# Optimization experiments

Measured on AMD Instinct MI355X. Metric: run time of the kernel, lower is better.

Reference implementation:

```python
import jax, jax.numpy as jnp
import numpy as np

T, B, D = 2048, 16, 1024


def setup_inputs() -> dict:
    key = jax.random.key(0)
    ks = jax.random.split(key, 8)
    std = 1.0 / D ** 0.5
    x = jax.random.normal(ks[0], (T, B, D), dtype=jnp.float32)
    h0 = jnp.zeros((B, D), dtype=jnp.float32)
    Wx = jax.random.uniform(ks[1], (D, D), jnp.float32, -std, std)
    R = jax.random.uniform(ks[2], (D, D), jnp.float32, -std, std)
    bias = jnp.zeros((D,), dtype=jnp.float32)
    W_delta = jax.random.uniform(ks[3], (D, D), jnp.float32, -std * 0.1, std * 0.1)
    b_delta = jnp.full((D,), 3.0, dtype=jnp.float32)  # delta_init
    A = jax.random.uniform(ks[4], (D,), jnp.float32, -0.5, 0.5)  # A_init_range
    W_gate_x = jax.random.uniform(ks[5], (D, D), jnp.float32, -std, std)
    W_gate_h = jax.random.uniform(ks[6], (D, D), jnp.float32, -std, std)
    b_gate = jnp.zeros((D,), dtype=jnp.float32)
    return {"x": x, "h0": h0, "Wx": Wx, "R": R, "bias": bias,
            "W_delta": W_delta, "b_delta": b_delta, "A": A,
            "W_gate_x": W_gate_x, "W_gate_h": W_gate_h, "b_gate": b_gate}


def reference(x, h0, Wx, R, bias, W_delta, b_delta, A, W_gate_x, W_gate_h, b_gate):
    # Input-dependent timestep: dt = softplus(x @ W_delta^T + b_delta), [T,B,D]
    dt = jax.nn.softplus(jnp.einsum('tbd,ed->tbe', x, W_delta) + b_delta)
    # Mamba-style log parameterization: decay_rate in (0,1), alpha in (0,1)
    decay_rate = jnp.exp(-jnp.exp(A))                 # [D]
    alpha = jnp.exp(-dt * decay_rate)                 # [T,B,D]
    # Precompute input projection once (big GEMM outside the scan)
    wx = jnp.einsum('tbd,ed->tbe', x, Wx) + bias      # [T,B,D]

    def step(h, inp):
        wx_t, a_t = inp                               # [B,D], [B,D]
        cand = jnp.tanh(h @ R.T + wx_t)               # nonlinear candidate
        h_new = a_t * h + (1.0 - a_t) * cand          # exponential blend
        return h_new, h_new

    _, h_out = jax.lax.scan(step, h0, (wx, alpha))    # h_out: [T,B,D] == h[1:]

    # h+x selective output gate
    gate_raw = (jnp.einsum('tbd,ed->tbe', x, W_gate_x)
                + jnp.einsum('tbd,ed->tbe', h_out, W_gate_h) + b_gate)
    return h_out * jax.nn.silu(gate_raw)
```

## Files before the change

### kernel.cpp

```cpp
#include <hip/hip_runtime.h>
#include <cstdint>
#include <cstddef>

typedef _Float16 f16;
typedef _Float16 f16x8 __attribute__((ext_vector_type(8)));
typedef _Float16 f16x4v __attribute__((ext_vector_type(4)));
typedef float f32x4 __attribute__((ext_vector_type(4)));
typedef unsigned uint2v __attribute__((ext_vector_type(2)));

#define TT 2048
#define BB 16
#define DD 1024
#define MM (TT*BB)
#define FPAD 16

__global__ void cvt_kernel(const float* __restrict__ in, f16* __restrict__ out, int n4){
  int stride = gridDim.x * blockDim.x;
  for (int j = blockIdx.x*blockDim.x + threadIdx.x; j < n4; j += stride){
    float4 v = ((const float4*)in)[j];
    f16x4v o;
    o[0]=(f16)v.x; o[1]=(f16)v.y; o[2]=(f16)v.z; o[3]=(f16)v.w;
    ((f16x4v*)out)[j] = o;
  }
}

__global__ void cvt5_kernel(const float* __restrict__ a0, const float* __restrict__ a1,
                            const float* __restrict__ a2, const float* __restrict__ a3,
                            const float* __restrict__ a4,
                            f16* __restrict__ o0, f16* __restrict__ o1,
                            f16* __restrict__ o2, f16* __restrict__ o3, f16* __restrict__ o4){
  const float* src[5] = {a0,a1,a2,a3,a4};
  f16* dst[5] = {o0,o1,o2,o3,o4};
  int which = blockIdx.y;
  const float* in = src[which];
  f16* out = dst[which];
  int j = blockIdx.x*blockDim.x + threadIdx.x;
  float4 v = ((const float4*)in)[j];
  f16x4v o;
  o[0]=(f16)v.x; o[1]=(f16)v.y; o[2]=(f16)v.z; o[3]=(f16)v.w;
  ((f16x4v*)out)[j] = o;
}

__global__ void init_rec_kernel(const float* __restrict__ h0, f16* __restrict__ hbuf,
                                unsigned* __restrict__ flags){
  int tid = blockIdx.x*blockDim.x + threadIdx.x;
  if (tid < 64*FPAD) flags[tid] = 0u;
  if (tid < BB*DD) hbuf[tid] = (f16)h0[tid];
}

#define GEMM_PROLOGUE() \
  __shared__ f16 As[128*32]; \
  __shared__ f16 Bs[128*32]; \
  int tid = threadIdx.x; \
  int l = tid & 63, w = tid >> 6; \
  int wr = w >> 1, wc = w & 1; \
  f32x4 acc[4][4]; \
  _Pragma("unroll") for (int i=0;i<4;++i) _Pragma("unroll") for (int jj=0;jj<4;++jj) \
    acc[i][jj] = (f32x4){0.f,0.f,0.f,0.f};

#define GEMM_KSTEP(Asrc, Bsrc, ktl) { \
  __syncthreads(); \
  _Pragma("unroll") for (int hh=0; hh<2; ++hh){ \
    int r = hh*64 + (tid>>2); \
    int q = (tid&3) ^ (r&3); \
    const f16* ga = (Asrc) + (size_t)(bm*128+r)*DD + (ktl)*32 + q*8; \
    const f16* gb = (Bsrc) + (size_t)(bcol*128+r)*DD + (ktl)*32 + q*8; \
    __builtin_amdgcn_global_load_lds((__attribute__((address_space(1))) void*)ga, \
        (__attribute__((address_space(3))) void*)(As + hh*2048 + tid*8), 16, 0, 0); \
    __builtin_amdgcn_global_load_lds((__attribute__((address_space(1))) void*)gb, \
        (__attribute__((address_space(3))) void*)(Bs + hh*2048 + tid*8), 16, 0, 0); \
  } \
  __syncthreads(); \
  int lr = l & 15, g = l >> 4; \
  f16x8 af[4], bf[4]; \
  _Pragma("unroll") for (int i=0;i<4;++i){ \
    int Ra = wr*64 + i*16 + lr; \
    int Rb = wc*64 + i*16 + lr; \
    af[i] = *(const f16x8*)(As + Ra*32 + ((g ^ (Ra & 3)) * 8)); \
    bf[i] = *(const f16x8*)(Bs + Rb*32 + ((g ^ (Rb & 3)) * 8)); \
  } \
  _Pragma("unroll") for (int i=0;i<4;++i) \
    _Pragma("unroll") for (int jj=0;jj<4;++jj) \
      acc[i][jj] = __builtin_amdgcn_mfma_f32_16x16x32_f16(af[i], bf[jj], acc[i][jj], 0,0,0); \
}

__global__ __launch_bounds__(256)
void gemm_wa_kernel(const f16* __restrict__ x16,
                    const f16* __restrict__ Wx16, const f16* __restrict__ Wd16,
                    f16* __restrict__ wxo, f16* __restrict__ alo,
                    const float* __restrict__ bias, const float* __restrict__ bd,
                    const float* __restrict__ Aar)
{
  int bm = blockIdx.x, bn = blockIdx.y;
  int alpha_path = (bn >= 8);
  int bcol = bn & 7;
  const f16* Bw = alpha_path ? Wd16 : Wx16;

  GEMM_PROLOGUE();
  for (int kt = 0; kt < 32; ++kt) GEMM_KSTEP(x16, Bw, kt);

  int lr = l & 15, lh = l >> 4;
  #pragma unroll
  for (int i=0;i<4;++i){
    #pragma unroll
    for (int jj=0;jj<4;++jj){
      #pragma unroll
      for (int r=0;r<4;++r){
        int row = bm*128 + wr*64 + i*16 + lh*4 + r;
        int col = bcol*128 + wc*64 + jj*16 + lr;
        float v = acc[i][jj][r];
        size_t off = (size_t)row*DD + col;
        if (!alpha_path){
          wxo[off] = (f16)(v + bias[col]);
        } else {
          float pre = v + bd[col];
          float sp  = (pre > 20.f) ? pre : log1pf(expf(pre));
          float decay = expf(-expf(Aar[col]));
          alo[off] = (f16)expf(-sp*decay);
        }
      }
    }
  }
}

__global__ __launch_bounds__(256)
void gemm_fin_kernel(const f16* __restrict__ hout16, const f16* __restrict__ x16,
                     const f16* __restrict__ Wgh16, const f16* __restrict__ Wgx16,
                     float* __restrict__ out, const float* __restrict__ bg)
{
  int bm = blockIdx.x, bcol = blockIdx.y;

  GEMM_PROLOGUE();
  for (int kt = 0; kt < 32; ++kt) GEMM_KSTEP(hout16, Wgh16, kt);
  for (int kt = 0; kt < 32; ++kt) GEMM_KSTEP(x16,    Wgx16, kt);

  int lr = l & 15, lh = l >> 4;
  #pragma unroll
  for (int i=0;i<4;++i){
    #pragma unroll
    for (int jj=0;jj<4;++jj){
      #pragma unroll
      for (int r=0;r<4;++r){
        int row = bm*128 + wr*64 + i*16 + lh*4 + r;
        int col = bcol*128 + wc*64 + jj*16 + lr;
        float g = acc[i][jj][r] + bg[col];
        size_t off = (size_t)row*DD + col;
        float hval = (float)hout16[off];
        out[off] = hval * g / (1.f + expf(-g));
      }
    }
  }
}

__global__ __launch_bounds__(64)
void rec_kernel(const f16* __restrict__ Rf, const f16* __restrict__ wx,
                const f16* __restrict__ alpha, const float* __restrict__ h0,
                f16* __restrict__ hbuf, f16* __restrict__ hout,
                unsigned* __restrict__ flags)
{
  __shared__ f16 Rlds[32*64*8];

  int l = threadIdx.x;
  int j = blockIdx.x;
  int e0 = j * 16;

  #pragma unroll
  for (int kt=0; kt<32; ++kt){
    int e = e0 + (l & 15);
    int d = kt*32 + (l >> 4)*8;
    *(uint4*)(Rlds + ((size_t)kt*64 + l)*8) = *(const uint4*)(Rf + (size_t)e*DD + d);
  }

  int b = l & 15, rr0 = (l >> 4) * 4;
  float4 hstate = *(const float4*)(h0 + (size_t)b*DD + e0 + rr0);
  __syncthreads();

  f32x4 wxv, alv;
  {
    f16x4v wh = *(const f16x4v*)(wx + (size_t)b*DD + e0 + rr0);
    f16x4v ah = *(const f16x4v*)(alpha + (size_t)b*DD + e0 + rr0);
    #pragma unroll
    for (int r=0;r<4;++r){ wxv[r] = (float)wh[r]; alv[r] = (float)ah[r]; }
  }

  for (int t = 0; t < TT; ++t){
    if (t > 0){
      const unsigned* fp = flags + l*FPAD;
      int guard = 0;
      unsigned long long notready = 1ull;
      while (notready && guard < 2000000){
        unsigned fv = __hip_atomic_load(fp, __ATOMIC_RELAXED, __HIP_MEMORY_SCOPE_AGENT);
        notready = __ballot(fv < (unsigned)t);
        ++guard;
        if (notready && guard > 16) __builtin_amdgcn_s_sleep(1);
      }
    }

    const f16* hb = hbuf + (size_t)(t & 1) * (BB*DD);
    f16x8 hfr[32];
    #pragma unroll
    for (int kt=0; kt<32; ++kt){
      const f16* hp = hb + (size_t)b*DD + kt*32 + (l >> 4)*8;
      asm volatile("global_load_dwordx4 %0, %1, off sc0 sc1"
                   : "=v"(hfr[kt]) : "v"(hp) : "memory");
    }

    f32x4 accv[4];
    #pragma unroll
    for (int c=0;c<4;++c) accv[c] = (f32x4){0.f,0.f,0.f,0.f};

    asm volatile("s_waitcnt vmcnt(24)" ::: "memory");
    __builtin_amdgcn_sched_barrier(0);
    #pragma unroll
    for (int kt=0; kt<8; ++kt){
      f16x8 a = *(const f16x8*)(Rlds + ((size_t)kt*64 + l)*8);
      accv[kt&3] = __builtin_amdgcn_mfma_f32_16x16x32_f16(a, hfr[kt], accv[kt&3], 0, 0, 0);
    }
    asm volatile("s_waitcnt vmcnt(16)" ::: "memory");
    __builtin_amdgcn_sched_barrier(0);
    #pragma unroll
    for (int kt=8; kt<16; ++kt){
      f16x8 a = *(const f16x8*)(Rlds + ((size_t)kt*64 + l)*8);
      accv[kt&3] = __builtin_amdgcn_mfma_f32_16x16x32_f16(a, hfr[kt], accv[kt&3], 0, 0, 0);
    }
    asm volatile("s_waitcnt vmcnt(8)" ::: "memory");
    __builtin_amdgcn_sched_barrier(0);

    int tn = (t+1 < TT) ? (t+1) : t;
    size_t offn = ((size_t)tn*BB + b)*DD + e0 + rr0;
    f16x4v whn = *(const f16x4v*)(wx + offn);
    f16x4v ahn = *(const f16x4v*)(alpha + offn);

    #pragma unroll
    for (int kt=16; kt<24; ++kt){
      f16x8 a = *(const f16x8*)(Rlds + ((size_t)kt*64 + l)*8);
      accv[kt&3] = __builtin_amdgcn_mfma_f32_16x16x32_f16(a, hfr[kt], accv[kt&3], 0, 0, 0);
    }
    asm volatile("s_waitcnt vmcnt(0)" ::: "memory");
    __builtin_amdgcn_sched_barrier(0);
    #pragma unroll
    for (int kt=24; kt<32; ++kt){
      f16x8 a = *(const f16x8*)(Rlds + ((size_t)kt*64 + l)*8);
      accv[kt&3] = __builtin_amdgcn_mfma_f32_16x16x32_f16(a, hfr[kt], accv[kt&3], 0, 0, 0);
    }
    f32x4 acc = (accv[0]+accv[1]) + (accv[2]+accv[3]);

    f16x4v h4;
    float hs[4] = {hstate.x, hstate.y, hstate.z, hstate.w};
    #pragma unroll
    for (int r=0;r<4;++r){
      float z = acc[r] + wxv[r];
      float cand = tanhf(z);
      float hn = alv[r]*hs[r] + (1.f - alv[r])*cand;
      hs[r] = hn;
      h4[r] = (f16)hn;
    }
    hstate = (float4){hs[0], hs[1], hs[2], hs[3]};

    f16* hw = hbuf + (size_t)((t+1) & 1) * (BB*DD) + (size_t)b*DD + e0 + rr0;
    uint2v hv = __builtin_bit_cast(uint2v, h4);
    asm volatile("global_store_dwordx2 %0, %1, off sc0 sc1"
                 :: "v"(hw), "v"(hv) : "memory");
    asm volatile("s_waitcnt vmcnt(0)" ::: "memory");
    if (l == 0)
      __hip_atomic_store(flags + j*FPAD, (unsigned)(t+1),
                         __ATOMIC_RELAXED, __HIP_MEMORY_SCOPE_AGENT);

    *(f16x4v*)(hout + ((size_t)t*BB + b)*DD + e0 + rr0) = h4;
    #pragma unroll
    for (int r=0;r<4;++r){ wxv[r] = (float)whn[r]; alv[r] = (float)ahn[r]; }
  }
}

extern "C" void kernel_launch(void* const* d_in, const int* in_sizes, int n_in,
                              void* d_out, int out_size, void* d_ws, size_t ws_size,
                              hipStream_t stream)
{
  const float* x    = (const float*)d_in[0];
  const float* h0   = (const float*)d_in[1];
  const float* Wx   = (const float*)d_in[2];
  const float* R    = (const float*)d_in[3];
  const float* bias = (const float*)d_in[4];
  const float* Wd   = (const float*)d_in[5];
  const float* bd   = (const float*)d_in[6];
  const float* Aar  = (const float*)d_in[7];
  const float* Wgx  = (const float*)d_in[8];
  const float* Wgh  = (const float*)d_in[9];
  const float* bg   = (const float*)d_in[10];
  float* out = (float*)d_out;

  char* ws = (char*)d_ws;
  size_t off = 0;
  auto carve = [&](size_t bytes) -> void* {
    void* p = ws + off;
    off += (bytes + 255) & ~(size_t)255;
    return p;
  };
  f16* x16    = (f16*)carve((size_t)MM*DD*2);
  f16* Wx16   = (f16*)carve((size_t)DD*DD*2);
  f16* Wd16   = (f16*)carve((size_t)DD*DD*2);
  f16* Wgx16  = (f16*)carve((size_t)DD*DD*2);
  f16* Wgh16  = (f16*)carve((size_t)DD*DD*2);
  f16* R16    = (f16*)carve((size_t)DD*DD*2);
  f16* wx16   = (f16*)carve((size_t)MM*DD*2);
  f16* al16   = (f16*)carve((size_t)MM*DD*2);
  f16* hout16 = (f16*)carve((size_t)MM*DD*2);
  f16* hbuf   = (f16*)carve((size_t)2*BB*DD*2);
  unsigned* flags = (unsigned*)carve(64*FPAD*4);
  if (off > ws_size) return;

  cvt_kernel<<<1024, 256, 0, stream>>>(x, x16, MM*DD/4);
  dim3 g5(DD*DD/4/256, 5);
  cvt5_kernel<<<g5, 256, 0, stream>>>(Wx, Wd, Wgx, Wgh, R,
                                      Wx16, Wd16, Wgx16, Wgh16, R16);
  init_rec_kernel<<<64, 256, 0, stream>>>(h0, hbuf, flags);

  dim3 gwa(MM/128, 16);
  gemm_wa_kernel<<<gwa, 256, 0, stream>>>(x16, Wx16, Wd16, wx16, al16, bias, bd, Aar);

  rec_kernel<<<64, 64, 0, stream>>>(R16, wx16, al16, h0, hbuf, hout16, flags);

  dim3 gfin(MM/128, DD/128);
  gemm_fin_kernel<<<gfin, 256, 0, stream>>>(hout16, x16, Wgh16, Wgx16, out, bg);
}
```

Before: 7.009 ms.

## Fuse recurrence with output-gate GEMM using persistent tile workers gated on progress

Merges the sequential recurrence kernel and the final gate GEMM into one launch. 64 blocks run the scan and publish a global step counter, while 192 persistent blocks pull output tiles from an atomic queue and start each tile once the rows of h it needs have been written. This overlaps the final GEMM with the latency-bound recurrence instead of running it afterwards. The cost is extra coherent (sc0 sc1) loads of hout, spin-waiting workers that may compete with the recurrence blocks for memory and CU resources, and a dependence on all blocks being co-resident.

Result: slower. 7.400 ms (+5.6%).

```diff
diff --git a/kernel.cpp b/kernel.cpp
--- a/kernel.cpp
+++ b/kernel.cpp
@@ -13,6 +13,10 @@
 #define DD 1024
 #define MM (TT*BB)
 #define FPAD 16
+#define NFIN 192
+
+#define AS1 __attribute__((address_space(1)))
+#define AS3 __attribute__((address_space(3)))
 
 __global__ void cvt_kernel(const float* __restrict__ in, f16* __restrict__ out, int n4){
   int stride = gridDim.x * blockDim.x;
@@ -44,7 +48,7 @@
 __global__ void init_rec_kernel(const float* __restrict__ h0, f16* __restrict__ hbuf,
                                 unsigned* __restrict__ flags){
   int tid = blockIdx.x*blockDim.x + threadIdx.x;
-  if (tid < 64*FPAD) flags[tid] = 0u;
+  if (tid < 64*FPAD + 64) flags[tid] = 0u;
   if (tid < BB*DD) hbuf[tid] = (f16)h0[tid];
 }
 
@@ -65,10 +69,8 @@
     int q = (tid&3) ^ (r&3); \
     const f16* ga = (Asrc) + (size_t)(bm*128+r)*DD + (ktl)*32 + q*8; \
     const f16* gb = (Bsrc) + (size_t)(bcol*128+r)*DD + (ktl)*32 + q*8; \
-    __builtin_amdgcn_global_load_lds((__attribute__((address_space(1))) void*)ga, \
-        (__attribute__((address_space(3))) void*)(As + hh*2048 + tid*8), 16, 0, 0); \
-    __builtin_amdgcn_global_load_lds((__attribute__((address_space(1))) void*)gb, \
-        (__attribute__((address_space(3))) void*)(Bs + hh*2048 + tid*8), 16, 0, 0); \
+    __builtin_amdgcn_global_load_lds((AS1 void*)ga, (AS3 void*)(As + hh*2048 + tid*8), 16, 0, 0); \
+    __builtin_amdgcn_global_load_lds((AS1 void*)gb, (AS3 void*)(Bs + hh*2048 + tid*8), 16, 0, 0); \
   } \
   __syncthreads(); \
   int lr = l & 15, g = l >> 4; \
@@ -124,151 +126,277 @@
 }
 
 __global__ __launch_bounds__(256)
-void gemm_fin_kernel(const f16* __restrict__ hout16, const f16* __restrict__ x16,
-                     const f16* __restrict__ Wgh16, const f16* __restrict__ Wgx16,
-                     float* __restrict__ out, const float* __restrict__ bg)
+void recfin_kernel(const f16* __restrict__ Rf, const f16* __restrict__ wx,
+                   const f16* __restrict__ alpha, const float* __restrict__ h0,
+                   f16* __restrict__ hbuf, f16* __restrict__ hout,
+                   unsigned* __restrict__ flags, unsigned* __restrict__ gstep,
+                   unsigned* __restrict__ wcnt,
+                   const f16* __restrict__ x16, const f16* __restrict__ Wgh16,
+                   const f16* __restrict__ Wgx16, float* __restrict__ out,
+                   const float* __restrict__ bg)
 {
-  int bm = blockIdx.x, bcol = blockIdx.y;
-
-  GEMM_PROLOGUE();
-  for (int kt = 0; kt < 32; ++kt) GEMM_KSTEP(hout16, Wgh16, kt);
-  for (int kt = 0; kt < 32; ++kt) GEMM_KSTEP(x16,    Wgx16, kt);
-
-  int lr = l & 15, lh = l >> 4;
-  #pragma unroll
-  for (int i=0;i<4;++i){
+  __shared__ __align__(16) char smem[32768];
+  __shared__ unsigned tilevar;
+
+  if (blockIdx.x < 64){
+    if (threadIdx.x >= 64) return;
+    f16* Rlds = (f16*)smem;
+    int l = threadIdx.x;
+    int j = blockIdx.x;
+    int e0 = j * 16;
+
     #pragma unroll
-    for (int jj=0;jj<4;++jj){
+    for (int kt=0; kt<32; ++kt){
+      int e = e0 + (l & 15);
+      int d = kt*32 + (l >> 4)*8;
+      *(uint4*)(Rlds + ((size_t)kt*64 + l)*8) = *(const uint4*)(Rf + (size_t)e*DD + d);
+    }
+    asm volatile("s_waitcnt lgkmcnt(0)" ::: "memory");
+    __builtin_amdgcn_sched_barrier(0);
+
+    int b = l & 15, rr0 = (l >> 4) * 4;
+    float4 hstate = *(const float4*)(h0 + (size_t)b*DD + e0 + rr0);
+
+    f32x4 wxv, alv;
+    {
+      f16x4v wh = *(const f16x4v*)(wx + (size_t)b*DD + e0 + rr0);
+      f16x4v ah = *(const f16x4v*)(alpha + (size_t)b*DD + e0 + rr0);
+      #pragma unroll
+      for (int r=0;r<4;++r){ wxv[r] = (float)wh[r]; alv[r] = (float)ah[r]; }
+    }
+
+    for (int t = 0; t < TT; ++t){
+      if (t > 0){
+        const unsigned* fp = flags + l*FPAD;
+        int guard = 0;
+        unsigned long long notready = 1ull;
+        while (notready && guard < 2000000){
+          unsigned fv = __hip_atomic_load(fp, __ATOMIC_RELAXED, __HIP_MEMORY_SCOPE_AGENT);
+          notready = __ballot(fv < (unsigned)t);
+          ++guard;
+          if (notready && guard > 16) __builtin_amdgcn_s_sleep(1);
+        }
+        if (j == 0 && l == 0)
+          __hip_atomic_store(gstep, (unsigned)t, __ATOMIC_RELAXED, __HIP_MEMORY_SCOPE_AGENT);
+      }
+
+      const f16* hb = hbuf + (size_t)(t & 1) * (BB*DD);
+      f16x8 hfr[32];
+      #pragma unroll
+      for (int kt=0; kt<32; ++kt){
+        const f16* hp = hb + (size_t)b*DD + kt*32 + (l >> 4)*8;
+        asm volatile("global_load_dwordx4 %0, %1, off sc0 sc1"
+                     : "=v"(hfr[kt]) : "v"(hp) : "memory");
+      }
+
+      f32x4 accv[4];
+      #pragma unroll
+      for (int c=0;c<4;++c) accv[c] = (f32x4){0.f,0.f,0.f,0.f};
+
+      asm volatile("s_waitcnt vmcnt(24)" ::: "memory");
+      __builtin_amdgcn_sched_barrier(0);
+      #pragma unroll
+      for (int kt=0; kt<8; ++kt){
+        f16x8 a = *(const f16x8*)(Rlds + ((size_t)kt*64 + l)*8);
+        accv[kt&3] = __builtin_amdgcn_mfma_f32_16x16x32_f16(a, hfr[kt], accv[kt&3], 0, 0, 0);
+      }
+      asm volatile("s_waitcnt vmcnt(16)" ::: "memory");
+      __builtin_amdgcn_sched_barrier(0);
+      #pragma unroll
+      for (int kt=8; kt<16; ++kt){
+        f16x8 a = *(const f16x8*)(Rlds + ((size_t)kt*64 + l)*8);
+        accv[kt&3] = __builtin_amdgcn_mfma_f32_16x16x32_f16(a, hfr[kt], accv[kt&3], 0, 0, 0);
+      }
+      asm volatile("s_waitcnt vmcnt(8)" ::: "memory");
+      __builtin_amdgcn_sched_barrier(0);
+
+      int tn = (t+1 < TT) ? (t+1) : t;
+      size_t offn = ((size_t)tn*BB + b)*DD + e0 + rr0;
+      f16x4v whn = *(const f16x4v*)(wx + offn);
+      f16x4v ahn = *(const f16x4v*)(alpha + offn);
+
+      #pragma unroll
+      for (int kt=16; kt<24; ++kt){
+        f16x8 a = *(const f16x8*)(Rlds + ((size_t)kt*64 + l)*8);
+        accv[kt&3] = __builtin_amdgcn_mfma_f32_16x16x32_f16(a, hfr[kt], accv[kt&3], 0, 0, 0);
+      }
+      asm volatile("s_waitcnt vmcnt(0)" ::: "memory");
+      __builtin_amdgcn_sched_barrier(0);
+      #pragma unroll
+      for (int kt=24; kt<32; ++kt){
+        f16x8 a = *(const f16x8*)(Rlds + ((size_t)kt*64 + l)*8);
+        accv[kt&3] = __builtin_amdgcn_mfma_f32_16x16x32_f16(a, hfr[kt], accv[kt&3], 0, 0, 0);
+      }
+      f32x4 acc = (accv[0]+accv[1]) + (accv[2]+accv[3]);
+
+      f16x4v h4;
+      float hs[4] = {hstate.x, hstate.y, hstate.z, hstate.w};
       #pragma unroll
       for (int r=0;r<4;++r){
-        int row = bm*128 + wr*64 + i*16 + lh*4 + r;
-        int col = bcol*128 + wc*64 + jj*16 + lr;
-        float g = acc[i][jj][r] + bg[col];
-        size_t off = (size_t)row*DD + col;
-        float hval = (float)hout16[off];
-        out[off] = hval * g / (1.f + expf(-g));
-      }
-    }
-  }
-}
-
-__global__ __launch_bounds__(64)
-void rec_kernel(const f16* __restrict__ Rf, const f16* __restrict__ wx,
-                const f16* __restrict__ alpha, const float* __restrict__ h0,
-                f16* __restrict__ hbuf, f16* __restrict__ hout,
-                unsigned* __restrict__ flags)
-{
-  __shared__ f16 Rlds[32*64*8];
-
-  int l = threadIdx.x;
-  int j = blockIdx.x;
-  int e0 = j * 16;
-
-  #pragma unroll
-  for (int kt=0; kt<32; ++kt){
-    int e = e0 + (l & 15);
-    int d = kt*32 + (l >> 4)*8;
-    *(uint4*)(Rlds + ((size_t)kt*64 + l)*8) = *(const uint4*)(Rf + (size_t)e*DD + d);
-  }
-
-  int b = l & 15, rr0 = (l >> 4) * 4;
-  float4 hstate = *(const float4*)(h0 + (size_t)b*DD + e0 + rr0);
-  __syncthreads();
-
-  f32x4 wxv, alv;
-  {
-    f16x4v wh = *(const f16x4v*)(wx + (size_t)b*DD + e0 + rr0);
-    f16x4v ah = *(const f16x4v*)(alpha + (size_t)b*DD + e0 + rr0);
-    #pragma unroll
-    for (int r=0;r<4;++r){ wxv[r] = (float)wh[r]; alv[r] = (float)ah[r]; }
-  }
-
-  for (int t = 0; t < TT; ++t){
-    if (t > 0){
+        float z = acc[r] + wxv[r];
+        float cand = tanhf(z);
+        float hn = alv[r]*hs[r] + (1.f - alv[r])*cand;
+        hs[r] = hn;
+        h4[r] = (f16)hn;
+      }
+      hstate = (float4){hs[0], hs[1], hs[2], hs[3]};
+
+      f16* hw = hbuf + (size_t)((t+1) & 1) * (BB*DD) + (size_t)b*DD + e0 + rr0;
+      uint2v hv = __builtin_bit_cast(uint2v, h4);
+      asm volatile("global_store_dwordx2 %0, %1, off sc0 sc1"
+                   :: "v"(hw), "v"(hv) : "memory");
+      f16* hop = hout + ((size_t)t*BB + b)*DD + e0 + rr0;
+      asm volatile("global_store_dwordx2 %0, %1, off sc0 sc1"
+                   :: "v"(hop), "v"(hv) : "memory");
+      asm volatile("s_waitcnt vmcnt(0)" ::: "memory");
+      if (l == 0)
+        __hip_atomic_store(flags + j*FPAD, (unsigned)(t+1),
+                           __ATOMIC_RELAXED, __HIP_MEMORY_SCOPE_AGENT);
+
+      #pragma unroll
+      for (int r=0;r<4;++r){ wxv[r] = (float)whn[r]; alv[r] = (float)ahn[r]; }
+    }
+
+    if (j == 0){
       const unsigned* fp = flags + l*FPAD;
       int guard = 0;
       unsigned long long notready = 1ull;
       while (notready && guard < 2000000){
         unsigned fv = __hip_atomic_load(fp, __ATOMIC_RELAXED, __HIP_MEMORY_SCOPE_AGENT);
-        notready = __ballot(fv < (unsigned)t);
+        notready = __ballot(fv < 2048u);
         ++guard;
-        if (notready && guard > 16) __builtin_amdgcn_s_sleep(1);
-      }
-    }
-
-    const f16* hb = hbuf + (size_t)(t & 1) * (BB*DD);
-    f16x8 hfr[32];
+        if (notready) __builtin_amdgcn_s_sleep(1);
+      }
+      if (l == 0)
+        __hip_atomic_store(gstep, 2048u, __ATOMIC_RELAXED, __HIP_MEMORY_SCOPE_AGENT);
+    }
+    return;
+  }
+
+  f16* As = (f16*)smem;
+  f16* Bs = (f16*)(smem + 8192);
+  int tid = threadIdx.x;
+  int l = tid & 63, w = tid >> 6;
+  int wr = w >> 1, wc = w & 1;
+  int lr = l & 15, lh = l >> 4;
+
+  for (;;){
+    if (tid == 0) tilevar = atomicAdd(wcnt, 1u);
+    __syncthreads();
+    unsigned g = tilevar;
+    __syncthreads();
+    if (g >= 2048u) break;
+    int bm = (int)(g >> 3), bcol = (int)(g & 7);
+
+    if (tid == 0){
+      unsigned need = (unsigned)((bm + 1) * 8);
+      int guard = 0;
+      while (guard < 1000000){
+        unsigned gs = __hip_atomic_load(gstep, __ATOMIC_RELAXED, __HIP_MEMORY_SCOPE_AGENT);
+        if (gs >= need) break;
+        ++guard;
+        __builtin_amdgcn_s_sleep(32);
+      }
+    }
+    __syncthreads();
+
+    f32x4 acc[4][4];
     #pragma unroll
-    for (int kt=0; kt<32; ++kt){
-      const f16* hp = hb + (size_t)b*DD + kt*32 + (l >> 4)*8;
-      asm volatile("global_load_dwordx4 %0, %1, off sc0 sc1"
-                   : "=v"(hfr[kt]) : "v"(hp) : "memory");
-    }
-
-    f32x4 accv[4];
+    for (int i=0;i<4;++i)
+      #pragma unroll
+      for (int jj=0;jj<4;++jj)
+        acc[i][jj] = (f32x4){0.f,0.f,0.f,0.f};
+
+    for (int kt = 0; kt < 32; ++kt){
+      __syncthreads();
+      int r0_ = tid >> 2,        q0 = (tid & 3) ^ (r0_ & 3);
+      int r1_ = 64 + (tid >> 2), q1 = (tid & 3) ^ (r1_ & 3);
+      f16x8 va0, va1;
+      const f16* ga0 = hout + (size_t)(bm*128 + r0_)*DD + kt*32 + q0*8;
+      const f16* ga1 = hout + (size_t)(bm*128 + r1_)*DD + kt*32 + q1*8;
+      asm volatile("global_load_dwordx4 %0, %1, off sc0 sc1" : "=v"(va0) : "v"(ga0) : "memory");
+      asm volatile("global_load_dwordx4 %0, %1, off sc0 sc1" : "=v"(va1) : "v"(ga1) : "memory");
+      const f16* gb0 = Wgh16 + (size_t)(bcol*128 + r0_)*DD + kt*32 + q0*8;
+      const f16* gb1 = Wgh16 + (size_t)(bcol*128 + r1_)*DD + kt*32 + q1*8;
+      __builtin_amdgcn_global_load_lds((AS1 void*)gb0, (AS3 void*)(Bs + tid*8), 16, 0, 0);
+      __builtin_amdgcn_global_load_lds((AS1 void*)gb1, (AS3 void*)(Bs + 2048 + tid*8), 16, 0, 0);
+      asm volatile("s_waitcnt vmcnt(0)" ::: "memory");
+      __builtin_amdgcn_sched_barrier(0);
+      *(f16x8*)(As + tid*8) = va0;
+      *(f16x8*)(As + 2048 + tid*8) = va1;
+      __syncthreads();
+      f16x8 af[4], bf[4];
+      #pragma unroll
+      for (int i=0;i<4;++i){
+        int Ra = wr*64 + i*16 + lr;
+        int Rb = wc*64 + i*16 + lr;
+        af[i] = *(const f16x8*)(As + Ra*32 + ((lh ^ (Ra & 3)) * 8));
+        bf[i] = *(const f16x8*)(Bs + Rb*32 + ((lh ^ (Rb & 3)) * 8));
+      }
+      #pragma unroll
+      for (int i=0;i<4;++i)
+        #pragma unroll
+        for (int jj=0;jj<4;++jj)
+          acc[i][jj] = __builtin_amdgcn_mfma_f32_16x16x32_f16(af[i], bf[jj], acc[i][jj], 0,0,0);
+    }
+
+    for (int kt = 0; kt < 32; ++kt){
+      __syncthreads();
+      #pragma unroll
+      for (int hh=0; hh<2; ++hh){
+        int r = hh*64 + (tid>>2);
+        int q = (tid&3) ^ (r&3);
+        const f16* ga = x16   + (size_t)(bm*128+r)*DD + kt*32 + q*8;
+        const f16* gb = Wgx16 + (size_t)(bcol*128+r)*DD + kt*32 + q*8;
+        __builtin_amdgcn_global_load_lds((AS1 void*)ga, (AS3 void*)(As + hh*2048 + tid*8), 16, 0, 0);
+        __builtin_amdgcn_global_load_lds((AS1 void*)gb, (AS3 void*)(Bs + hh*2048 + tid*8), 16, 0, 0);
+      }
+      __syncthreads();
+      f16x8 af[4], bf[4];
+      #pragma unroll
+      for (int i=0;i<4;++i){
+        int Ra = wr*64 + i*16 + lr;
+        int Rb = wc*64 + i*16 + lr;
+        af[i] = *(const f16x8*)(As + Ra*32 + ((lh ^ (Ra & 3)) * 8));
+        bf[i] = *(const f16x8*)(Bs + Rb*32 + ((lh ^ (Rb & 3)) * 8));
+      }
+      #pragma unroll
+      for (int i=0;i<4;++i)
+        #pragma unroll
+        for (int jj=0;jj<4;++jj)
+          acc[i][jj] = __builtin_amdgcn_mfma_f32_16x16x32_f16(af[i], bf[jj], acc[i][jj], 0,0,0);
+    }
+
+    unsigned hvr[4][4][4];
     #pragma unroll
-    for (int c=0;c<4;++c) accv[c] = (f32x4){0.f,0.f,0.f,0.f};
-
-    asm volatile("s_waitcnt vmcnt(24)" ::: "memory");
-    __builtin_amdgcn_sched_barrier(0);
-    #pragma unroll
-    for (int kt=0; kt<8; ++kt){
-      f16x8 a = *(const f16x8*)(Rlds + ((size_t)kt*64 + l)*8);
-      accv[kt&3] = __builtin_amdgcn_mfma_f32_16x16x32_f16(a, hfr[kt], accv[kt&3], 0, 0, 0);
-    }
-    asm volatile("s_waitcnt vmcnt(16)" ::: "memory");
-    __builtin_amdgcn_sched_barrier(0);
-    #pragma unroll
-    for (int kt=8; kt<16; ++kt){
-      f16x8 a = *(const f16x8*)(Rlds + ((size_t)kt*64 + l)*8);
-      accv[kt&3] = __builtin_amdgcn_mfma_f32_16x16x32_f16(a, hfr[kt], accv[kt&3], 0, 0, 0);
-    }
-    asm volatile("s_waitcnt vmcnt(8)" ::: "memory");
-    __builtin_amdgcn_sched_barrier(0);
-
-    int tn = (t+1 < TT) ? (t+1) : t;
-    size_t offn = ((size_t)tn*BB + b)*DD + e0 + rr0;
-    f16x4v whn = *(const f16x4v*)(wx + offn);
-    f16x4v ahn = *(const f16x4v*)(alpha + offn);
-
-    #pragma unroll
-    for (int kt=16; kt<24; ++kt){
-      f16x8 a = *(const f16x8*)(Rlds + ((size_t)kt*64 + l)*8);
-      accv[kt&3] = __builtin_amdgcn_mfma_f32_16x16x32_f16(a, hfr[kt], accv[kt&3], 0, 0, 0);
-    }
+    for (int i=0;i<4;++i)
+      #pragma unroll
+      for (int jj=0;jj<4;++jj)
+        #pragma unroll
+        for (int r=0;r<4;++r){
+          const f16* hp = hout + (size_t)(bm*128 + wr*64 + i*16 + lh*4 + r)*DD
+                               + bcol*128 + wc*64 + jj*16 + lr;
+          asm volatile("global_load_ushort %0, %1, off sc0 sc1"
+                       : "=v"(hvr[i][jj][r]) : "v"(hp) : "memory");
+        }
     asm volatile("s_waitcnt vmcnt(0)" ::: "memory");
     __builtin_amdgcn_sched_barrier(0);
+
     #pragma unroll
-    for (int kt=24; kt<32; ++kt){
-      f16x8 a = *(const f16x8*)(Rlds + ((size_t)kt*64 + l)*8);
-      accv[kt&3] = __builtin_amdgcn_mfma_f32_16x16x32_f16(a, hfr[kt], accv[kt&3], 0, 0, 0);
-    }
-    f32x4 acc = (accv[0]+accv[1]) + (accv[2]+accv[3]);
-
-    f16x4v h4;
-    float hs[4] = {hstate.x, hstate.y, hstate.z, hstate.w};
-    #pragma unroll
-    for (int r=0;r<4;++r){
-      float z = acc[r] + wxv[r];
-      float cand = tanhf(z);
-      float hn = alv[r]*hs[r] + (1.f - alv[r])*cand;
-      hs[r] = hn;
-      h4[r] = (f16)hn;
-    }
-    hstate = (float4){hs[0], hs[1], hs[2], hs[3]};
-
-    f16* hw = hbuf + (size_t)((t+1) & 1) * (BB*DD) + (size_t)b*DD + e0 + rr0;
-    uint2v hv = __builtin_bit_cast(uint2v, h4);
-    asm volatile("global_store_dwordx2 %0, %1, off sc0 sc1"
-                 :: "v"(hw), "v"(hv) : "memory");
-    asm volatile("s_waitcnt vmcnt(0)" ::: "memory");
-    if (l == 0)
-      __hip_atomic_store(flags + j*FPAD, (unsigned)(t+1),
-                         __ATOMIC_RELAXED, __HIP_MEMORY_SCOPE_AGENT);
-
-    *(f16x4v*)(hout + ((size_t)t*BB + b)*DD + e0 + rr0) = h4;
-    #pragma unroll
-    for (int r=0;r<4;++r){ wxv[r] = (float)whn[r]; alv[r] = (float)ahn[r]; }
+    for (int i=0;i<4;++i){
+      #pragma unroll
+      for (int jj=0;jj<4;++jj){
+        #pragma unroll
+        for (int r=0;r<4;++r){
+          int row = bm*128 + wr*64 + i*16 + lh*4 + r;
+          int col = bcol*128 + wc*64 + jj*16 + lr;
+          float gg = acc[i][jj][r] + bg[col];
+          unsigned short us = (unsigned short)hvr[i][jj][r];
+          float hval = (float)__builtin_bit_cast(f16, us);
+          out[(size_t)row*DD + col] = hval * gg / (1.f + expf(-gg));
+        }
+      }
+    }
   }
 }
 
@@ -306,7 +434,9 @@
   f16* al16   = (f16*)carve((size_t)MM*DD*2);
   f16* hout16 = (f16*)carve((size_t)MM*DD*2);
   f16* hbuf   = (f16*)carve((size_t)2*BB*DD*2);
-  unsigned* flags = (unsigned*)carve(64*FPAD*4);
+  unsigned* flags = (unsigned*)carve((64*FPAD + 64)*4);
+  unsigned* gstep = flags + 64*FPAD;
+  unsigned* wcnt  = flags + 64*FPAD + 32;
   if (off > ws_size) return;
 
   cvt_kernel<<<1024, 256, 0, stream>>>(x, x16, MM*DD/4);
@@ -318,8 +448,7 @@
   dim3 gwa(MM/128, 16);
   gemm_wa_kernel<<<gwa, 256, 0, stream>>>(x16, Wx16, Wd16, wx16, al16, bias, bd, Aar);
 
-  rec_kernel<<<64, 64, 0, stream>>>(R16, wx16, al16, h0, hbuf, hout16, flags);
-
-  dim3 gfin(MM/128, DD/128);
-  gemm_fin_kernel<<<gfin, 256, 0, stream>>>(hout16, x16, Wgh16, Wgx16, out, bg);
-}
+  recfin_kernel<<<64 + NFIN, 256, 0, stream>>>(R16, wx16, al16, h0, hbuf, hout16,
+                                               flags, gstep, wcnt,
+                                               x16, Wgh16, Wgx16, out, bg);
+}
```
